# Kernel optimization log

Hardware: AMD Instinct MI355X
Metric: run time of the kernel (lower is better)

## Reference

```python
import jax, jax.numpy as jnp
import numpy as np


def _lrelu(x):
    return jnp.where(x >= 0, x, 0.2 * x)


def _mod_conv(x, style, w_mod, weight, stride, demodulate):
    # x: (B, Cin, H, W); style: (B, S); w_mod: (Cin, S); weight: (Cout, Cin, k, k)
    B, Cin, H, W = x.shape
    Cout, _, k, _ = weight.shape
    scale = 1.0 / np.sqrt(Cin * k * k)
    s = style @ w_mod.T                                   # (B, Cin) per-sample modulation
    w = scale * weight[None] * s[:, None, :, None, None]  # (B, Cout, Cin, k, k)
    if demodulate:
        d = jax.lax.rsqrt(jnp.sum(w * w, axis=(2, 3, 4)) + 1e-8)
        w = w * d[:, :, None, None, None]
    w = w.reshape(B * Cout, Cin, k, k)
    xr = x.reshape(1, B * Cin, H, W)
    pad = k // 2
    out = jax.lax.conv_general_dilated(
        xr, w, (stride, stride), [(pad, pad), (pad, pad)],
        dimension_numbers=('NCHW', 'OIHW', 'NCHW'), feature_group_count=B)
    return out.reshape(B, Cout, out.shape[2], out.shape[3])


def _mapping(z, labels, emb, map_W, map_b, map_g, map_beta):
    x = z + emb[labels]
    for i in range(map_W.shape[0]):
        x = x @ map_W[i].T + map_b[i]
        mu = jnp.mean(x, axis=0)
        var = jnp.var(x, axis=0)  # biased, as torch BatchNorm uses for normalization
        x = (x - mu) * jax.lax.rsqrt(var + 1e-5) * map_g[i] + map_beta[i]
        x = _lrelu(x)
    return x


def _block(x, w, c1w, c1m, c2w, c2m, n1w, n2w, na, nb):
    x = _mod_conv(x, w, c1m, c1w, 1, True)
    x = _lrelu(x + n1w[None, :, None, None] * na)
    x = _mod_conv(x, w, c2m, c2w, 2, True)  # up=2 -> stride=2 strided conv (as in source)
    x = _lrelu(x + n2w[None, :, None, None] * nb)
    return x


def setup_inputs() -> dict:
    key = jax.random.key(0)
    ks = iter(jax.random.split(key, 64))
    nrm = lambda shape, s=1.0: jax.random.normal(next(ks), shape, jnp.float32) * s
    B, Z, Wd, L, LAB = 8, 512, 512, 8, 10
    inp = {}
    inp['z'] = nrm((B, Z))
    inp['labels'] = jax.random.randint(next(ks), (B,), 0, LAB)
    inp['emb'] = nrm((LAB, Z), 0.1)
    inp['map_W'] = nrm((L, Wd, Z), float(np.sqrt(2.0 / Z)))
    inp['map_b'] = jnp.zeros((L, Wd), jnp.float32)
    inp['map_g'] = jnp.ones((L, Wd), jnp.float32)
    inp['map_beta'] = jnp.zeros((L, Wd), jnp.float32)
    inp['const'] = nrm((128, 256, 256))
    inp['b1c1_w'] = nrm((128, 128, 3, 3)); inp['b1c1_m'] = nrm((128, Wd), 0.04)
    inp['b1c2_w'] = nrm((128, 128, 3, 3)); inp['b1c2_m'] = nrm((128, Wd), 0.04)
    inp['b1n1_w'] = nrm((128,), 0.1); inp['b1n2_w'] = nrm((128,), 0.1)
    inp['b2c1_w'] = nrm((64, 128, 3, 3)); inp['b2c1_m'] = nrm((128, Wd), 0.04)
    inp['b2c2_w'] = nrm((64, 64, 3, 3)); inp['b2c2_m'] = nrm((64, Wd), 0.04)
    inp['b2n1_w'] = nrm((64,), 0.1); inp['b2n2_w'] = nrm((64,), 0.1)
    inp['b3c1_w'] = nrm((32, 64, 3, 3)); inp['b3c1_m'] = nrm((64, Wd), 0.04)
    inp['b3c2_w'] = nrm((32, 32, 3, 3)); inp['b3c2_m'] = nrm((32, Wd), 0.04)
    inp['b3n1_w'] = nrm((32,), 0.1); inp['b3n2_w'] = nrm((32,), 0.1)
    inp['rgb_w'] = nrm((1, 32, 1, 1)); inp['rgb_m'] = nrm((32, Wd), 0.04)
    inp['n1a'] = nrm((B, 1, 256, 256)); inp['n1b'] = nrm((B, 1, 128, 128))
    inp['n2a'] = nrm((B, 1, 128, 128)); inp['n2b'] = nrm((B, 1, 64, 64))
    inp['n3a'] = nrm((B, 1, 64, 64)); inp['n3b'] = nrm((B, 1, 32, 32))
    return inp


def reference(z, labels, emb, map_W, map_b, map_g, map_beta, const,
              b1c1_w, b1c1_m, b1c2_w, b1c2_m, b1n1_w, b1n2_w,
              b2c1_w, b2c1_m, b2c2_w, b2c2_m, b2n1_w, b2n2_w,
              b3c1_w, b3c1_m, b3c2_w, b3c2_m, b3n1_w, b3n2_w,
              rgb_w, rgb_m, n1a, n1b, n2a, n2b, n3a, n3b):
    B = z.shape[0]
    w = _mapping(z, labels, emb, map_W, map_b, map_g, map_beta)
    x = jnp.broadcast_to(const[None], (B,) + const.shape)
    x = _block(x, w, b1c1_w, b1c1_m, b1c2_w, b1c2_m, b1n1_w, b1n2_w, n1a, n1b)
    x = _block(x, w, b2c1_w, b2c1_m, b2c2_w, b2c2_m, b2n1_w, b2n2_w, n2a, n2b)
    x = _block(x, w, b3c1_w, b3c1_m, b3c2_w, b3c2_m, b3n1_w, b3n2_w, n3a, n3b)
    # final block: F.interpolate(..., size=(256,240), mode='bilinear', align_corners=False)
    x = jax.image.resize(x, (B, x.shape[1], 256, 240), method='bilinear')
    out = _mod_conv(x, w, rgb_m, rgb_w, 1, False)  # to-grayscale 1x1, no demod
    return out
```

## Files before the change

### kernel.cpp

```cpp
#include <hip/hip_runtime.h>
#include <hip/hip_bf16.h>


typedef __hip_bfloat16 bf16;
typedef __attribute__((ext_vector_type(8))) short bf16x8;
typedef __attribute__((ext_vector_type(4))) float f32x4;

__device__ __forceinline__ float b2f(bf16 v){ return __bfloat162float(v); }
__device__ __forceinline__ bf16  f2b(float v){ return __float2bfloat16(v); }
__device__ __forceinline__ unsigned short bbits(float v){
  bf16 h = f2b(v); union { bf16 h; unsigned short u; } x; x.h = h; return x.u;
}
__device__ __forceinline__ float ldf(const void* p, size_t i, int isf32){
  return isf32 ? ((const float*)p)[i] : b2f(((const bf16*)p)[i]);
}
__device__ __forceinline__ void stf(void* p, size_t i, int isf32, float v){
  if (isf32) ((float*)p)[i] = v; else ((bf16*)p)[i] = f2b(v);
}

__global__ __launch_bounds__(256) void detect_dtype(const unsigned short* __restrict__ cst,
    int* __restrict__ flag){
  __shared__ int cnt[256];
  int t = threadIdx.x, c = 0;
  for (int i=t; i<4096; i+=256){
    unsigned short w = cst[i];
    int mag = w & 0x7FFF;
    int e = mag >> 7;
    if (mag == 0 || (e >= 96 && e <= 150)) c++;
  }
  cnt[t] = c; __syncthreads();
  for (int s=128; s>0; s>>=1){ if (t<s) cnt[t] += cnt[t+s]; __syncthreads(); }
  if (t == 0) *flag = (cnt[0] >= 3500) ? 0 : 1;
}

__global__ __launch_bounds__(256) void cvt_const(const void* __restrict__ cst,
    short* __restrict__ out, const int* __restrict__ dflag){
  int isf32 = *dflag;
  __shared__ __align__(16) short sh[64*136];
  int t = threadIdx.x;
  int p0 = blockIdx.x * 64;
  for (int i=t; i<128*64; i+=256){
    int ci = i >> 6, px = i & 63;
    float v = ldf(cst, (size_t)ci*65536 + p0 + px, isf32);
    sh[px*136 + ci] = (short)bbits(v);
  }
  __syncthreads();
  for (int i=t; i<64*16; i+=256){
    int px = i >> 4, c8 = (i & 15) * 8;
    bf16x8 val = *(const bf16x8*)&sh[px*136 + c8];
    *(bf16x8*)(out + ((size_t)(p0+px))*128 + c8) = val;
  }
}

__global__ __launch_bounds__(256) void map_init(const void* __restrict__ z,
    const int* __restrict__ labels, const void* __restrict__ emb,
    float* __restrict__ x0, const int* __restrict__ dflag){
  int isf32 = *dflag;
  int i = blockIdx.x*256 + threadIdx.x;
  int b = i >> 9, k = i & 511;
  x0[i] = ldf(z, i, isf32) + ldf(emb, (size_t)labels[b]*512 + k, isf32);
}

__global__ __launch_bounds__(64) void map_layer(const float* __restrict__ xin,
    float* __restrict__ xout, const void* __restrict__ W, size_t wOff,
    const void* __restrict__ bl, const void* __restrict__ gl,
    const void* __restrict__ betal, size_t vOff, const int* __restrict__ dflag){
  int isf32 = *dflag;
  int j = blockIdx.x;
  int l = threadIdx.x;
  int b = l >> 3, sp = l & 7;
  float part = 0.f;
  int k0 = sp*64;
  size_t wrow = wOff + (size_t)j*512 + k0;
  for (int k=0; k<64; k++)
    part += xin[b*512 + k0 + k] * ldf(W, wrow + k, isf32);
  part += __shfl_xor(part, 1);
  part += __shfl_xor(part, 2);
  part += __shfl_xor(part, 4);
  float y = part + ldf(bl, vOff + j, isf32);
  float ys[8];
  float mu = 0.f;
  #pragma unroll
  for (int bb=0; bb<8; bb++){ ys[bb] = __shfl(y, bb*8); mu += ys[bb]; }
  mu *= 0.125f;
  float var = 0.f;
  #pragma unroll
  for (int bb=0; bb<8; bb++){ float d = ys[bb]-mu; var += d*d; }
  var *= 0.125f;
  float xn = (y-mu)*rsqrtf(var+1e-5f)*ldf(gl, vOff + j, isf32) + ldf(betal, vOff + j, isf32);
  xn = (xn >= 0.f) ? xn : 0.2f*xn;
  if (sp == 0) xout[b*512 + j] = xn;
}

__global__ __launch_bounds__(64) void styles_kernel(const float* __restrict__ w,
    float* __restrict__ s_all,
    const void* m0, const void* m1, const void* m2, const void* m3,
    const void* m4, const void* m5, const void* m6, const int* __restrict__ dflag){
  int isf32 = *dflag;
  int id = blockIdx.x;
  const int offs[8] = {0,1024,2048,3072,3584,4096,4352,4608};
  const int cins[7] = {128,128,128,64,64,32,32};
  const void* ms[7] = {m0,m1,m2,m3,m4,m5,m6};
  int c = 0;
  while (id >= offs[c+1]) c++;
  int r = id - offs[c];
  int Cin = cins[c];
  int b = r / Cin, ci = r % Cin;
  int l = threadIdx.x;
  float acc = 0.f;
  for (int k=l; k<512; k+=64) acc += w[b*512 + k] * ldf(ms[c], (size_t)ci*512 + k, isf32);
  #pragma unroll
  for (int m=1; m<64; m<<=1) acc += __shfl_xor(acc, m);
  if (l == 0) s_all[id] = acc;
}

__global__ __launch_bounds__(64) void modw_kernel(const float* __restrict__ s_all,
    bf16* __restrict__ wmod,
    const void* w0, const void* w1, const void* w2, const void* w3,
    const void* w4, const void* w5, const void* w6, const int* __restrict__ dflag){
  int isf32 = *dflag;
  int bid = blockIdx.x;
  int base, Cout, Cin, soff, wmoff, demod = 1;
  const void* wp;
  if      (bid < 1024){ base=0;    Cout=128; Cin=128; soff=0;    wmoff=0;       wp=w0; }
  else if (bid < 2048){ base=1024; Cout=128; Cin=128; soff=1024; wmoff=1179648; wp=w1; }
  else if (bid < 2560){ base=2048; Cout=64;  Cin=128; soff=2048; wmoff=2359296; wp=w2; }
  else if (bid < 3072){ base=2560; Cout=64;  Cin=64;  soff=3072; wmoff=2949120; wp=w3; }
  else if (bid < 3328){ base=3072; Cout=32;  Cin=64;  soff=3584; wmoff=3244032; wp=w4; }
  else if (bid < 3584){ base=3328; Cout=32;  Cin=32;  soff=4096; wmoff=3391488; wp=w5; }
  else                { base=3584; Cout=1;   Cin=32;  soff=4352; wmoff=3465216; wp=w6; demod=0; }
  int kk = demod ? 9 : 1;
  int L  = Cin * kk;
  int bc = bid - base;
  int b  = bc / Cout, co = bc % Cout;
  float scale = 1.0f / sqrtf((float)L);
  int l = threadIdx.x;
  float part = 0.f;
  for (int e=l; e<L; e+=64){
    int ci = e / kk;
    float v = scale * ldf(wp, (size_t)co*L + e, isf32) * s_all[soff + b*Cin + ci];
    part += v*v;
  }
  #pragma unroll
  for (int m=1; m<64; m<<=1) part += __shfl_xor(part, m);
  float d = demod ? rsqrtf(part + 1e-8f) : 1.0f;
  for (int e=l; e<L; e+=64){
    int ci = e / kk, tap = e % kk;
    float v = scale * ldf(wp, (size_t)co*L + e, isf32) * s_all[soff + b*Cin + ci];
    size_t idx;
    if (demod){
      int c32 = ci >> 5;
      int lane2 = ((ci >> 3) & 3) * 16 + (co & 15);
      int j = ci & 7;
      int mtg = co >> 4;
      idx = (size_t)wmoff +
            ((((size_t)b*9 + tap)*(Cin>>5) + c32)*(Cout>>4) + mtg)*512 + lane2*8 + j;
    } else {
      idx = (size_t)wmoff + (size_t)b*Cin + e;
    }
    wmod[idx] = f2b(v * d);
  }
}

template<int MT, int NT, int S>
__global__ __launch_bounds__(256) void convmf(
    const short* __restrict__ X, long long xbs, int Cin, int Hin, int Win,
    const bf16* __restrict__ WA, const void* __restrict__ noise,
    const void* __restrict__ nwp, short* __restrict__ Y, long long ybs,
    int Cout, int Hout, int Wout, int wtile, int nrowsOut,
    const int* __restrict__ dflag){
  int isf32 = *dflag;
  const int W_in_t = (S==1) ? (wtile+2) : (2*wtile+1);
  const int R_in   = (S==1) ? (nrowsOut+2) : (2*nrowsOut+1);
  __shared__ __align__(16) short act[15600];
  int t = threadIdx.x;
  int lane = t & 63, wv = t >> 6;
  int mw = wv & 1, nwv = wv >> 1;
  int lanelow = lane & 15, quad = lane >> 4;
  int tiles_x = Wout / wtile;
  int tx = blockIdx.x % tiles_x, ty = blockIdx.x / tiles_x;
  int ox0 = tx * wtile, oy0 = ty * nrowsOut;
  int iy0 = S*oy0 - 1, ix0 = S*ox0 - 1;
  int z = blockIdx.z;
  const short* Xb = X + (size_t)z * xbs;
  short* Yb = Y + (size_t)z * ybs;
  const int Cin32 = Cin >> 5, Cout16 = Cout >> 4;
  const bf16x8* WAimg = (const bf16x8*)WA + (size_t)z * 9 * Cin32 * Cout16 * 64;
  f32x4 acc[MT][NT];
  #pragma unroll
  for (int mt=0; mt<MT; mt++)
    #pragma unroll
    for (int nt=0; nt<NT; nt++) acc[mt][nt] = (f32x4){0.f,0.f,0.f,0.f};
  int rowb[NT], xb[NT];
  #pragma unroll
  for (int nt=0; nt<NT; nt++){
    int nl = nwv*NT*16 + nt*16;
    rowb[nt] = nl / wtile;
    xb[nt]  = nl % wtile + lanelow;
  }
  for (int c32=0; c32<Cin32; c32++){
    int c0 = c32 << 5;
    __syncthreads();
    for (int i=t; i<R_in*W_in_t; i+=256){
      int r = i / W_in_t, x = i % W_in_t;
      int gy = iy0 + r, gx = ix0 + x;
      bf16x8* dst = (bf16x8*)&act[i*40];
      if (gy>=0 && gy<Hin && gx>=0 && gx<Win){
        const bf16x8* src = (const bf16x8*)(Xb + ((size_t)gy*Win + gx)*Cin + c0);
        dst[0]=src[0]; dst[1]=src[1]; dst[2]=src[2]; dst[3]=src[3];
      } else {
        bf16x8 zz = (bf16x8){0,0,0,0,0,0,0,0};
        dst[0]=zz; dst[1]=zz; dst[2]=zz; dst[3]=zz;
      }
    }
    __syncthreads();
    #pragma unroll
    for (int tap=0; tap<9; tap++){
      int ky = tap/3, kx = tap%3;
      bf16x8 afr[MT], bfr[NT];
      #pragma unroll
      for (int mt=0; mt<MT; mt++){
        int mtg = mw*MT + mt;
        afr[mt] = WAimg[(((size_t)tap*Cin32 + c32)*Cout16 + mtg)*64 + lane];
      }
      #pragma unroll
      for (int nt=0; nt<NT; nt++){
        int off = ((S*rowb[nt] + ky)*W_in_t + (S*xb[nt] + kx))*40 + quad*8;
        bfr[nt] = *(const bf16x8*)&act[off];
      }
      #pragma unroll
      for (int mt=0; mt<MT; mt++)
        #pragma unroll
        for (int nt=0; nt<NT; nt++)
          acc[mt][nt] = __builtin_amdgcn_mfma_f32_16x16x32_bf16(
              afr[mt], bfr[nt], acc[mt][nt], 0, 0, 0);
    }
  }
  #pragma unroll
  for (int nt=0; nt<NT; nt++){
    int oy = oy0 + rowb[nt], ox = ox0 + xb[nt];
    float nv = ldf(noise, ((size_t)z*Hout + oy)*Wout + ox, isf32);
    #pragma unroll
    for (int mt=0; mt<MT; mt++){
      int co0 = (mw*MT + mt)*16 + quad*4;
      ushort4 pk;
      float v0 = acc[mt][nt][0] + ldf(nwp, co0+0, isf32)*nv; v0 = (v0>=0.f)?v0:0.2f*v0;
      float v1 = acc[mt][nt][1] + ldf(nwp, co0+1, isf32)*nv; v1 = (v1>=0.f)?v1:0.2f*v1;
      float v2 = acc[mt][nt][2] + ldf(nwp, co0+2, isf32)*nv; v2 = (v2>=0.f)?v2:0.2f*v2;
      float v3 = acc[mt][nt][3] + ldf(nwp, co0+3, isf32)*nv; v3 = (v3>=0.f)?v3:0.2f*v3;
      pk.x = bbits(v0); pk.y = bbits(v1); pk.z = bbits(v2); pk.w = bbits(v3);
      *(ushort4*)&Yb[((size_t)oy*Wout + ox)*Cout + co0] = pk;
    }
  }
}

__global__ __launch_bounds__(256) void resize_rgb(const short* __restrict__ X,
    long long xbs, const bf16* __restrict__ wr, void* __restrict__ out,
    const int* __restrict__ dflag){
  int isf32 = *dflag;
  int b = blockIdx.y;
  const short* Xb = X + (size_t)b * xbs;
  int i = blockIdx.x*256 + threadIdx.x;
  int x = i % 240;
  int y = i / 240;
  float sy = (y + 0.5f)*0.125f - 0.5f;
  float sx = (x + 0.5f)*(32.0f/240.0f) - 0.5f;
  float y0f = floorf(sy), x0f = floorf(sx);
  float fy = sy - y0f, fx = sx - x0f;
  int y0 = (int)y0f, x0 = (int)x0f;
  int y1 = min(y0+1, 31), x1 = min(x0+1, 31);
  y0 = max(y0, 0); x0 = max(x0, 0);
  const short* p00 = Xb + ((size_t)(y0*32 + x0))*32;
  const short* p01 = Xb + ((size_t)(y0*32 + x1))*32;
  const short* p10 = Xb + ((size_t)(y1*32 + x0))*32;
  const short* p11 = Xb + ((size_t)(y1*32 + x1))*32;
  float w00 = (1.f-fy)*(1.f-fx), w01 = (1.f-fy)*fx, w10 = fy*(1.f-fx), w11 = fy*fx;
  float acc = 0.f;
  for (int ci=0; ci<32; ci++){
    float v = w00*b2f(((const bf16*)p00)[ci]) + w01*b2f(((const bf16*)p01)[ci])
            + w10*b2f(((const bf16*)p10)[ci]) + w11*b2f(((const bf16*)p11)[ci]);
    acc += b2f(wr[b*32 + ci]) * v;
  }
  stf(out, (size_t)b*61440 + i, isf32, acc);
}

extern "C" void kernel_launch(void* const* d_in, const int* in_sizes, int n_in,
                              void* d_out, int out_size, void* d_ws, size_t ws_size,
                              hipStream_t stream){
  const void* z        = d_in[0];
  const int*  labels   = (const int*)d_in[1];
  const void* emb      = d_in[2];
  const void* map_W    = d_in[3];
  const void* map_b    = d_in[4];
  const void* map_g    = d_in[5];
  const void* map_beta = d_in[6];
  const void* cst      = d_in[7];
  const void* cw0 = d_in[8];   const void* cm0 = d_in[9];
  const void* cw1 = d_in[10];  const void* cm1 = d_in[11];
  const void* n1w = d_in[12];  const void* n2w = d_in[13];
  const void* cw2 = d_in[14];  const void* cm2 = d_in[15];
  const void* cw3 = d_in[16];  const void* cm3 = d_in[17];
  const void* n3w = d_in[18];  const void* n4w = d_in[19];
  const void* cw4 = d_in[20];  const void* cm4 = d_in[21];
  const void* cw5 = d_in[22];  const void* cm5 = d_in[23];
  const void* n5w = d_in[24];  const void* n6w = d_in[25];
  const void* cw6 = d_in[26];  const void* cm6 = d_in[27];
  const void* n1a = d_in[28];  const void* n1b = d_in[29];
  const void* n2a = d_in[30];  const void* n2b = d_in[31];
  const void* n3a = d_in[32];  const void* n3b = d_in[33];

  int*   flag  = (int*)d_ws;
  float* xA    = (float*)((char*)d_ws + 256);
  float* xB    = (float*)((char*)d_ws + 16640);
  float* s_all = (float*)((char*)d_ws + 33024);
  bf16*  wmod  = (bf16*)((char*)d_ws + 51456);
  short* A1    = (short*)((char*)d_ws + 6983680);
  short* A2    = (short*)((char*)d_ws + 141201408);

  detect_dtype<<<1,256,0,stream>>>((const unsigned short*)cst, flag);
  cvt_const<<<1024,256,0,stream>>>(cst, A2, flag);
  map_init<<<16,256,0,stream>>>(z, labels, emb, xA, flag);
  float* cur = xA; float* nxt = xB;
  for (int l=0; l<8; l++){
    map_layer<<<512,64,0,stream>>>(cur, nxt, map_W, (size_t)l*512*512,
                                   map_b, map_g, map_beta, (size_t)l*512, flag);
    float* tmp = cur; cur = nxt; nxt = tmp;
  }
  styles_kernel<<<4608,64,0,stream>>>(cur, s_all, cm0, cm1, cm2, cm3, cm4, cm5, cm6, flag);
  modw_kernel<<<3592,64,0,stream>>>(s_all, wmod, cw0, cw1, cw2, cw3, cw4, cw5, cw6, flag);

  bf16* wm0 = wmod;
  bf16* wm1 = wmod + 1179648;
  bf16* wm2 = wmod + 2359296;
  bf16* wm3 = wmod + 2949120;
  bf16* wm4 = wmod + 3244032;
  bf16* wm5 = wmod + 3391488;
  bf16* wm6 = wmod + 3465216;

  const long long A1e  = 256LL*256*128;
  const long long A1Be = 128LL*128*128;
  const long long A2e  = 128LL*128*64;
  const long long A2Be = 64LL*64*64;
  const long long A3e  = 64LL*64*32;
  const long long A3Be = 32LL*32*32;

  convmf<4,4,1><<<dim3(512,1,8),256,0,stream>>>(A2, 0, 128, 256, 256,
      wm0, n1a, n1w, A1, A1e, 128, 256, 256, 128, 1, flag);
  convmf<4,2,2><<<dim3(256,1,8),256,0,stream>>>(A1, A1e, 128, 256, 256,
      wm1, n1b, n2w, A2, A1Be, 128, 128, 128, 64, 1, flag);
  convmf<2,4,1><<<dim3(128,1,8),256,0,stream>>>(A2, A1Be, 128, 128, 128,
      wm2, n2a, n3w, A1, A2e, 64, 128, 128, 128, 1, flag);
  convmf<2,2,2><<<dim3(64,1,8),256,0,stream>>>(A1, A2e, 64, 128, 128,
      wm3, n2b, n4w, A2, A2Be, 64, 64, 64, 64, 1, flag);
  convmf<1,4,1><<<dim3(32,1,8),256,0,stream>>>(A2, A2Be, 64, 64, 64,
      wm4, n3a, n5w, A1, A3e, 32, 64, 64, 64, 2, flag);
  convmf<1,2,2><<<dim3(16,1,8),256,0,stream>>>(A1, A3e, 32, 64, 64,
      wm5, n3b, n6w, A2, A3Be, 32, 32, 32, 32, 2, flag);
  resize_rgb<<<dim3(240,8),256,0,stream>>>(A2, A3Be, wm6, d_out, flag);
}
```

Baseline: 698.6 us.

## Double-buffer conv input tiles via register prefetch with quad-split LDS layout

The tile width and row count become template parameters, so tile sizes and index math are compile-time constants. The input tile is staged in LDS through a two-buffer scheme: the next 32-channel slice is loaded into registers while MFMAs run on the current one, then written to the other buffer. This replaces the two-barrier load-then-compute loop. The LDS layout changes from 40-short padded pixels to a quad-major split, with even and odd columns separated for stride 2, to change bank access patterns. The cost is more registers for staging and double the LDS footprint, which may lower occupancy.

Result: slower. 785.2 us (+12.4%).

```diff
diff --git a/kernel.cpp b/kernel.cpp
--- a/kernel.cpp
+++ b/kernel.cpp
@@ -162,24 +162,28 @@
   }
 }
 
-template<int MT, int NT, int S>
+template<int MT, int NT, int S, int WT, int NR>
 __global__ __launch_bounds__(256) void convmf(
     const short* __restrict__ X, long long xbs, int Cin, int Hin, int Win,
     const bf16* __restrict__ WA, const void* __restrict__ noise,
     const void* __restrict__ nwp, short* __restrict__ Y, long long ybs,
-    int Cout, int Hout, int Wout, int wtile, int nrowsOut,
-    const int* __restrict__ dflag){
-  int isf32 = *dflag;
-  const int W_in_t = (S==1) ? (wtile+2) : (2*wtile+1);
-  const int R_in   = (S==1) ? (nrowsOut+2) : (2*nrowsOut+1);
-  __shared__ __align__(16) short act[15600];
+    int Cout, int Hout, int Wout, const int* __restrict__ dflag){
+  constexpr int W_in_t = (S==1) ? (WT+2) : (2*WT+1);
+  constexpr int R_in   = (S==1) ? (NR+2) : (2*NR+1);
+  constexpr int ENT    = R_in * W_in_t;
+  constexpr int NEh    = (W_in_t+1)/2;
+  constexpr int ITEMS  = ENT*4;
+  constexpr int NIT    = (ITEMS + 255)/256;
+  constexpr int BUFE   = 4*ENT*8;
+  __shared__ __align__(16) short act[2*BUFE];
+  int isf32 = *dflag;
   int t = threadIdx.x;
   int lane = t & 63, wv = t >> 6;
   int mw = wv & 1, nwv = wv >> 1;
   int lanelow = lane & 15, quad = lane >> 4;
-  int tiles_x = Wout / wtile;
+  int tiles_x = Wout / WT;
   int tx = blockIdx.x % tiles_x, ty = blockIdx.x / tiles_x;
-  int ox0 = tx * wtile, oy0 = ty * nrowsOut;
+  int ox0 = tx*WT, oy0 = ty*NR;
   int iy0 = S*oy0 - 1, ix0 = S*ox0 - 1;
   int z = blockIdx.z;
   const short* Xb = X + (size_t)z * xbs;
@@ -195,25 +199,44 @@
   #pragma unroll
   for (int nt=0; nt<NT; nt++){
     int nl = nwv*NT*16 + nt*16;
-    rowb[nt] = nl / wtile;
-    xb[nt]  = nl % wtile + lanelow;
-  }
+    rowb[nt] = nl / WT;
+    xb[nt]  = nl % WT + lanelow;
+  }
+  bf16x8 stg[NIT];
+  auto loadregs = [&](int c32){
+    int c0 = c32 << 5;
+    #pragma unroll
+    for (int it=0; it<NIT; it++){
+      int i = it*256 + t;
+      if (i < ITEMS){
+        int e = i >> 2, q = i & 3;
+        int r = e / W_in_t, x = e - r*W_in_t;
+        int gy = iy0 + r, gx = ix0 + x;
+        if (gy>=0 && gy<Hin && gx>=0 && gx<Win)
+          stg[it] = *(const bf16x8*)(Xb + ((size_t)gy*Win + gx)*Cin + c0 + q*8);
+        else
+          stg[it] = (bf16x8){0,0,0,0,0,0,0,0};
+      }
+    }
+  };
+  auto writelds = [&](int buf){
+    #pragma unroll
+    for (int it=0; it<NIT; it++){
+      int i = it*256 + t;
+      if (i < ITEMS){
+        int e = i >> 2, q = i & 3;
+        int r = e / W_in_t, x = e - r*W_in_t;
+        int pos = (S==1) ? x : ((x>>1) + (x&1)*NEh);
+        *(bf16x8*)&act[(size_t)buf*BUFE + ((q*ENT) + r*W_in_t + pos)*8] = stg[it];
+      }
+    }
+  };
+  loadregs(0);
+  writelds(0);
   for (int c32=0; c32<Cin32; c32++){
-    int c0 = c32 << 5;
     __syncthreads();
-    for (int i=t; i<R_in*W_in_t; i+=256){
-      int r = i / W_in_t, x = i % W_in_t;
-      int gy = iy0 + r, gx = ix0 + x;
-      bf16x8* dst = (bf16x8*)&act[i*40];
-      if (gy>=0 && gy<Hin && gx>=0 && gx<Win){
-        const bf16x8* src = (const bf16x8*)(Xb + ((size_t)gy*Win + gx)*Cin + c0);
-        dst[0]=src[0]; dst[1]=src[1]; dst[2]=src[2]; dst[3]=src[3];
-      } else {
-        bf16x8 zz = (bf16x8){0,0,0,0,0,0,0,0};
-        dst[0]=zz; dst[1]=zz; dst[2]=zz; dst[3]=zz;
-      }
-    }
-    __syncthreads();
+    if (c32+1 < Cin32) loadregs(c32+1);
+    int bo = (c32 & 1) * BUFE;
     #pragma unroll
     for (int tap=0; tap<9; tap++){
       int ky = tap/3, kx = tap%3;
@@ -225,8 +248,10 @@
       }
       #pragma unroll
       for (int nt=0; nt<NT; nt++){
-        int off = ((S*rowb[nt] + ky)*W_in_t + (S*xb[nt] + kx))*40 + quad*8;
-        bfr[nt] = *(const bf16x8*)&act[off];
+        int row = S*rowb[nt] + ky;
+        int pos = (S==1) ? (xb[nt] + kx)
+                         : (xb[nt] + (kx>>1) + (kx&1)*NEh);
+        bfr[nt] = *(const bf16x8*)&act[bo + (quad*ENT + row*W_in_t + pos)*8];
       }
       #pragma unroll
       for (int mt=0; mt<MT; mt++)
@@ -235,6 +260,7 @@
           acc[mt][nt] = __builtin_amdgcn_mfma_f32_16x16x32_bf16(
               afr[mt], bfr[nt], acc[mt][nt], 0, 0, 0);
     }
+    if (c32+1 < Cin32) writelds((c32+1) & 1);
   }
   #pragma unroll
   for (int nt=0; nt<NT; nt++){
@@ -344,17 +370,17 @@
   const long long A3e  = 64LL*64*32;
   const long long A3Be = 32LL*32*32;
 
-  convmf<4,4,1><<<dim3(512,1,8),256,0,stream>>>(A2, 0, 128, 256, 256,
-      wm0, n1a, n1w, A1, A1e, 128, 256, 256, 128, 1, flag);
-  convmf<4,2,2><<<dim3(256,1,8),256,0,stream>>>(A1, A1e, 128, 256, 256,
-      wm1, n1b, n2w, A2, A1Be, 128, 128, 128, 64, 1, flag);
-  convmf<2,4,1><<<dim3(128,1,8),256,0,stream>>>(A2, A1Be, 128, 128, 128,
-      wm2, n2a, n3w, A1, A2e, 64, 128, 128, 128, 1, flag);
-  convmf<2,2,2><<<dim3(64,1,8),256,0,stream>>>(A1, A2e, 64, 128, 128,
-      wm3, n2b, n4w, A2, A2Be, 64, 64, 64, 64, 1, flag);
-  convmf<1,4,1><<<dim3(32,1,8),256,0,stream>>>(A2, A2Be, 64, 64, 64,
-      wm4, n3a, n5w, A1, A3e, 32, 64, 64, 64, 2, flag);
-  convmf<1,2,2><<<dim3(16,1,8),256,0,stream>>>(A1, A3e, 32, 64, 64,
-      wm5, n3b, n6w, A2, A3Be, 32, 32, 32, 32, 2, flag);
+  convmf<4,4,1,128,1><<<dim3(512,1,8),256,0,stream>>>(A2, 0, 128, 256, 256,
+      wm0, n1a, n1w, A1, A1e, 128, 256, 256, flag);
+  convmf<4,2,2,64,1><<<dim3(256,1,8),256,0,stream>>>(A1, A1e, 128, 256, 256,
+      wm1, n1b, n2w, A2, A1Be, 128, 128, 128, flag);
+  convmf<2,4,1,128,1><<<dim3(128,1,8),256,0,stream>>>(A2, A1Be, 128, 128, 128,
+      wm2, n2a, n3w, A1, A2e, 64, 128, 128, flag);
+  convmf<2,2,2,64,1><<<dim3(64,1,8),256,0,stream>>>(A1, A2e, 64, 128, 128,
+      wm3, n2b, n4w, A2, A2Be, 64, 64, 64, flag);
+  convmf<1,4,1,64,2><<<dim3(32,1,8),256,0,stream>>>(A2, A2Be, 64, 64, 64,
+      wm4, n3a, n5w, A1, A3e, 32, 64, 64, flag);
+  convmf<1,2,2,32,2><<<dim3(16,1,8),256,0,stream>>>(A1, A3e, 32, 64, 64,
+      wm5, n3b, n6w, A2, A3Be, 32, 32, 32, flag);
   resize_rgb<<<dim3(240,8),256,0,stream>>>(A2, A3Be, wm6, d_out, flag);
 }
```
